# Optimization experiments

Hardware: AMD Instinct MI355X
Metric: run time of the kernel (lower is better)

## Reference

```python
import jax, jax.numpy as jnp
import numpy as np

NUM_CLASSES = 10
OUTPUT_DIM = 128
HIDDEN_DIM = 64


def setup_inputs() -> dict:
    key = jax.random.key(0)
    k1, k2, k3, k4, k5, k6 = jax.random.split(key, 6)
    B, S, F = 16, 4096, 512
    X_support = jax.random.normal(k1, (B, S, F), dtype=jnp.float32)
    y_support = jax.random.randint(k2, (B, S), 0, NUM_CLASSES, dtype=jnp.int32)
    # MLP params: Linear(6, HIDDEN) -> GELU -> Linear(HIDDEN, OUTPUT)
    w1 = jax.random.normal(k3, (6, HIDDEN_DIM), dtype=jnp.float32) * (1.0 / np.sqrt(6.0))
    b1 = jax.random.normal(k4, (HIDDEN_DIM,), dtype=jnp.float32) * 0.01
    w2 = jax.random.normal(k5, (HIDDEN_DIM, OUTPUT_DIM), dtype=jnp.float32) * (1.0 / np.sqrt(HIDDEN_DIM))
    b2 = jax.random.normal(k6, (OUTPUT_DIM,), dtype=jnp.float32) * 0.01
    return {"X_support": X_support, "y_support": y_support,
            "w1": w1, "b1": b1, "w2": w2, "b2": b2}


def _feature_target_stats(X, y):
    """Vectorized equivalent of FeatureTargetStatsEncoder per-(batch,feature) loops.
    X: [B, S, F] float, y: [B, S] int class labels. Returns stats [B, F, 6]."""
    B, S, F = X.shape
    missing_rate = jnp.isnan(X).astype(X.dtype).mean(axis=1)           # [B, F]
    Xc = jnp.nan_to_num(X, nan=0.0)
    gmean = Xc.mean(axis=1)                                            # [B, F]
    variance = Xc.var(axis=1)                                          # biased (unbiased=False)
    absX = jnp.abs(Xc)
    mean_abs = absX.mean(axis=1)
    max_abs = absX.max(axis=1)
    # unique_ratio: count distinct values per (b, f) via sort + diff
    xs = jnp.sort(Xc, axis=1)
    n_unique = 1.0 + (jnp.diff(xs, axis=1) != 0).astype(Xc.dtype).sum(axis=1)
    unique_ratio = n_unique / S
    # classification target score: between-class variance / overall variance
    onehot = jax.nn.one_hot(y, NUM_CLASSES, dtype=Xc.dtype)            # [B, S, C]
    counts = onehot.sum(axis=1)                                        # [B, C]
    csum = jnp.einsum('bsc,bsf->bcf', onehot, Xc)                      # [B, C, F]
    cmean = csum / jnp.maximum(counts, 1.0)[:, :, None]
    dev2 = (cmean - gmean[:, None, :]) ** 2
    between = (counts[:, :, None] * dev2).sum(axis=1) / jnp.maximum(counts.sum(axis=1), 1.0)[:, None]
    target_score = between / jnp.maximum(variance, 1e-6)
    stats = jnp.stack([target_score, missing_rate, unique_ratio,
                       variance, mean_abs, max_abs], axis=-1)          # [B, F, 6]
    return jnp.nan_to_num(stats, nan=0.0, posinf=0.0, neginf=0.0)


def reference(X_support, y_support, w1, b1, w2, b2):
    stats = _feature_target_stats(X_support, y_support)                # [B, F, 6]
    h = jax.nn.gelu(stats @ w1 + b1, approximate=False)               # exact GELU like nn.GELU()
    return h @ w2 + b2                                                 # [B, F, OUTPUT_DIM]
```

## Files before the change

### kernel.cpp

```cpp
#include <hip/hip_runtime.h>
#include <math.h>

#define NS 4096
#define NF 512
#define NB 16
#define NC 10
#define HSIZE 8192
#define HMASK 8191
#define HEMPTY 0xFFFFFFFFu
#define TSR 128
#define TSC 16
#define NSEG 4
#define SEGR (NS / NSEG)
#define WS_P_OFF  1024
#define P2_BYTES (NB * NF * NSEG * 16 * 4)
#define WS_XT_OFF (WS_P_OFF + P2_BYTES)

__device__ __forceinline__ float wave_reduce_add(float v) {
    #pragma unroll
    for (int off = 32; off > 0; off >>= 1) v += __shfl_down(v, off, 64);
    return v;
}

__device__ __forceinline__ unsigned int pat_of(float x) {
    if (x != x) x = 0.f;
    unsigned int p = __float_as_uint(x);
    return (p == 0x80000000u) ? 0u : p;
}

__device__ __forceinline__ float resolve1(unsigned int* hash,
                                          unsigned int s, unsigned int p, unsigned int o) {
    if (o == HEMPTY) return 1.f;
    if (o == p)      return 0.f;
    for (;;) {
        s = (s + 1) & HMASK;
        const unsigned int oo = atomicCAS(&hash[s], HEMPTY, p);
        if (oo == HEMPTY) return 1.f;
        if (oo == p)      return 0.f;
    }
}

__device__ __forceinline__ float hash8(unsigned int* hash, const float4 u, const float4 v) {
    const unsigned int p0 = pat_of(u.x), p1 = pat_of(u.y), p2 = pat_of(u.z), p3 = pat_of(u.w);
    const unsigned int p4 = pat_of(v.x), p5 = pat_of(v.y), p6 = pat_of(v.z), p7 = pat_of(v.w);
    const unsigned int s0 = (p0 * 2654435761u) >> 19, s1 = (p1 * 2654435761u) >> 19;
    const unsigned int s2 = (p2 * 2654435761u) >> 19, s3 = (p3 * 2654435761u) >> 19;
    const unsigned int s4 = (p4 * 2654435761u) >> 19, s5 = (p5 * 2654435761u) >> 19;
    const unsigned int s6 = (p6 * 2654435761u) >> 19, s7 = (p7 * 2654435761u) >> 19;
    const unsigned int o0 = atomicCAS(&hash[s0], HEMPTY, p0);
    const unsigned int o1 = atomicCAS(&hash[s1], HEMPTY, p1);
    const unsigned int o2 = atomicCAS(&hash[s2], HEMPTY, p2);
    const unsigned int o3 = atomicCAS(&hash[s3], HEMPTY, p3);
    const unsigned int o4 = atomicCAS(&hash[s4], HEMPTY, p4);
    const unsigned int o5 = atomicCAS(&hash[s5], HEMPTY, p5);
    const unsigned int o6 = atomicCAS(&hash[s6], HEMPTY, p6);
    const unsigned int o7 = atomicCAS(&hash[s7], HEMPTY, p7);
    float u8 = 0.f;
    u8 += resolve1(hash, s0, p0, o0);
    u8 += resolve1(hash, s1, p1, o1);
    u8 += resolve1(hash, s2, p2, o2);
    u8 += resolve1(hash, s3, p3, o3);
    u8 += resolve1(hash, s4, p4, o4);
    u8 += resolve1(hash, s5, p5, o5);
    u8 += resolve1(hash, s6, p6, o6);
    u8 += resolve1(hash, s7, p7, o7);
    return u8;
}

__launch_bounds__(512, 4)
__global__ void stripe_stats_kernel(const float* __restrict__ X,
                                    float* __restrict__ XT,
                                    const int* __restrict__ y,
                                    float* __restrict__ P2,
                                    int* __restrict__ counts_i) {
    __shared__ float t[TSR][TSC + 1];
    __shared__ int ys[TSR];
    __shared__ int hist[NC];
    const int b   = blockIdx.x;
    const int f0  = blockIdx.y * TSC;
    const int seg = blockIdx.z;
    const int tid = threadIdx.x;
    const bool do_hist = (blockIdx.y == 0);
    if (do_hist && tid < NC) hist[tid] = 0;

    const int lrow = tid >> 2, lq = tid & 3;
    const int col  = tid >> 5, rq = tid & 31;

    const int sbase = seg * SEGR;
    const float* Xb = X + (size_t)b * NS * NF + f0 + lq * 4;
    const int*   yb = y + (size_t)b * NS;

    float sum = 0.f, sumsq = 0.f, sumabs = 0.f, maxabs = 0.f, nancnt = 0.f;
    float csum[NC];
    #pragma unroll
    for (int c = 0; c < NC; c++) csum[c] = 0.f;

    float4 xcur = *(const float4*)(Xb + (size_t)(sbase + lrow) * NF);
    int4 ycur = make_int4(0, 0, 0, 0);
    if (tid < TSR / 4) ycur = *(const int4*)(yb + sbase + tid * 4);

    for (int it = 0; it < SEGR / TSR; ++it) {
        const int s0 = sbase + it * TSR;
        float4 xnext = xcur; int4 ynext = ycur;
        if (it + 1 < SEGR / TSR) {
            xnext = *(const float4*)(Xb + (size_t)(s0 + TSR + lrow) * NF);
            if (tid < TSR / 4) ynext = *(const int4*)(yb + s0 + TSR + tid * 4);
        }
        __syncthreads();
        t[lrow][lq * 4 + 0] = xcur.x; t[lrow][lq * 4 + 1] = xcur.y;
        t[lrow][lq * 4 + 2] = xcur.z; t[lrow][lq * 4 + 3] = xcur.w;
        if (tid < TSR / 4) {
            ys[tid * 4 + 0] = ycur.x; ys[tid * 4 + 1] = ycur.y;
            ys[tid * 4 + 2] = ycur.z; ys[tid * 4 + 3] = ycur.w;
        }
        __syncthreads();
        if (do_hist && tid < TSR) atomicAdd(&hist[ys[tid]], 1);

        #pragma unroll
        for (int j = 0; j < 4; j++) {
            const int r = rq + 32 * j;
            float x = t[r][col];
            const int yc = ys[r];
            if (x != x) { nancnt += 1.f; x = 0.f; }
            sum += x;
            sumsq = fmaf(x, x, sumsq);
            const float a = fabsf(x);
            sumabs += a;
            maxabs = fmaxf(maxabs, a);
            #pragma unroll
            for (int c = 0; c < NC; c++) csum[c] += (yc == c) ? x : 0.f;
        }
        float4 wv;
        wv.x = t[rq * 4 + 0][col]; wv.y = t[rq * 4 + 1][col];
        wv.z = t[rq * 4 + 2][col]; wv.w = t[rq * 4 + 3][col];
        *(float4*)(XT + ((size_t)b * NF + f0 + col) * NS + s0 + rq * 4) = wv;

        xcur = xnext; ycur = ynext;
    }

    float st[15] = { sum, sumsq, sumabs, nancnt, maxabs,
                     csum[0], csum[1], csum[2], csum[3], csum[4],
                     csum[5], csum[6], csum[7], csum[8], csum[9] };
    #pragma unroll
    for (int s = 0; s < 15; s++) {
        float v = st[s];
        #pragma unroll
        for (int off = 16; off > 0; off >>= 1) {
            const float o = __shfl_down(v, off, 32);
            v = (s == 4) ? fmaxf(v, o) : v + o;
        }
        if (rq == 0)
            P2[(((size_t)b * NF + f0 + col) * NSEG + seg) * 16 + s] = v;
    }
    if (do_hist) {
        __syncthreads();
        if (tid < NC) atomicAdd(&counts_i[b * NC + tid], hist[tid]);
    }
}

__launch_bounds__(512, 8)
__global__ void fused_hash_mlp(const float* __restrict__ XT,
                               const float* __restrict__ P2,
                               const int* __restrict__ counts_i,
                               const float* __restrict__ w1,
                               const float* __restrict__ b1,
                               const float* __restrict__ w2,
                               const float* __restrict__ b2,
                               float* __restrict__ out) {
    __shared__ __align__(16) unsigned int hash[HSIZE];

    const int w = blockIdx.x;
    const int g = (w & 7) * 1024 + (w >> 3);
    const int b = g >> 9;
    const int f = g & (NF - 1);
    const int tid = threadIdx.x;
    const int wave = tid >> 6, lane = tid & 63;

    const float4* Xc4 = (const float4*)(XT + ((size_t)b * NF + f) * NS);
    const float4 xa = Xc4[tid];
    const float4 xb = Xc4[512 + tid];

    uint4* h4 = (uint4*)hash;
    const uint4 e4 = make_uint4(HEMPTY, HEMPTY, HEMPTY, HEMPTY);
    #pragma unroll
    for (int i = 0; i < HSIZE / 4 / 512; i++) h4[i * 512 + tid] = e4;
    __syncthreads();

    float uniq = hash8(hash, xa, xb);

    __syncthreads();

    float* r = (float*)hash;
    float* stats_s = r + 32;
    float* h_s = r + 64;

    uniq = wave_reduce_add(uniq);
    if (lane == 0) r[wave] = uniq;
    __syncthreads();

    if (tid == 0) {
        float u = 0.f;
        #pragma unroll
        for (int i = 0; i < 8; i++) u += r[i];
        const float* Pp = P2 + ((size_t)b * NF + f) * (NSEG * 16);
        float S[15];
        #pragma unroll
        for (int s = 0; s < 15; s++) {
            float v0 = Pp[s], v1 = Pp[16 + s], v2 = Pp[32 + s], v3 = Pp[48 + s];
            S[s] = (s == 4) ? fmaxf(fmaxf(v0, v1), fmaxf(v2, v3))
                            : (v0 + v1) + (v2 + v3);
        }
        const float invS = 1.f / (float)NS;
        const float gmean    = S[0] * invS;
        const float variance = fmaxf(S[1] * invS - gmean * gmean, 0.f);
        const float mean_abs = S[2] * invS;
        const float missing  = S[3] * invS;
        const float max_abs  = S[4];
        float between = 0.f;
        #pragma unroll
        for (int c = 0; c < NC; c++) {
            const float cnt = (float)counts_i[b * NC + c];
            const float cm  = S[5 + c] / fmaxf(cnt, 1.f);
            const float d   = cm - gmean;
            between = fmaf(cnt * d, d, between);
        }
        between *= invS;
        const float target = between / fmaxf(variance, 1e-6f);
        float st6[6] = { target, missing, u * invS, variance, mean_abs, max_abs };
        #pragma unroll
        for (int i = 0; i < 6; i++) {
            float v = st6[i];
            if (!(fabsf(v) < INFINITY)) v = 0.f;
            stats_s[i] = v;
        }
    }
    __syncthreads();

    if (tid < 64) {
        float z = b1[tid];
        #pragma unroll
        for (int i = 0; i < 6; i++) z = fmaf(stats_s[i], w1[i * 64 + tid], z);
        h_s[tid] = 0.5f * z * (1.f + erff(z * 0.70710678118654752440f));
    }
    __syncthreads();
    if (tid < 128) {
        float o = b2[tid];
        #pragma unroll
        for (int j = 0; j < 64; j++) o = fmaf(h_s[j], w2[j * 128 + tid], o);
        out[(size_t)g * 128 + tid] = o;
    }
}

__global__ void count_classes_kernel(const int* __restrict__ y, float* __restrict__ counts) {
    __shared__ int hist[NC];
    const int b = blockIdx.x;
    if (threadIdx.x < NC) hist[threadIdx.x] = 0;
    __syncthreads();
    for (int s = threadIdx.x; s < NS; s += blockDim.x)
        atomicAdd(&hist[y[b * NS + s]], 1);
    __syncthreads();
    if (threadIdx.x < NC) counts[b * NC + threadIdx.x] = (float)hist[threadIdx.x];
}

__device__ __forceinline__ float wave_reduce_add64(float v) {
    #pragma unroll
    for (int off = 32; off > 0; off >>= 1) v += __shfl_down(v, off, 64);
    return v;
}
__device__ __forceinline__ float wave_reduce_max64(float v) {
    #pragma unroll
    for (int off = 32; off > 0; off >>= 1) v = fmaxf(v, __shfl_down(v, off, 64));
    return v;
}

__launch_bounds__(256)
__global__ void fused_stats_mlp_kernel(const float* __restrict__ X,
                                       const int* __restrict__ y,
                                       const float* __restrict__ counts,
                                       const float* __restrict__ w1,
                                       const float* __restrict__ b1,
                                       const float* __restrict__ w2,
                                       const float* __restrict__ b2,
                                       float* __restrict__ out) {
    __shared__ unsigned int hash[HSIZE];
    __shared__ float red[4][16];
    __shared__ float stats_s[6];
    __shared__ float h_s[64];

    const int w = blockIdx.x;
    const int g = (w & 7) * 1024 + (w >> 3);
    const int b = g >> 9;
    const int f = g & (NF - 1);
    const int tid = threadIdx.x;

    #pragma unroll
    for (int i = 0; i < HSIZE / 256; i++) hash[tid + i * 256] = HEMPTY;
    __syncthreads();

    const float* Xp = X + (size_t)b * NS * NF + f;
    const int*   yp = y + b * NS;

    float sum = 0.f, sumsq = 0.f, sumabs = 0.f, maxabs = 0.f, nancnt = 0.f, uniq = 0.f;
    float csum[NC];
    #pragma unroll
    for (int c = 0; c < NC; c++) csum[c] = 0.f;

    #pragma unroll
    for (int k0 = 0; k0 < 16; k0 += 8) {
        float xv[8]; int yv[8];
        #pragma unroll
        for (int k = 0; k < 8; k++) {
            const int s = (k0 + k) * 256 + tid;
            xv[k] = Xp[(size_t)s * NF];
            yv[k] = yp[s];
        }
        #pragma unroll
        for (int k = 0; k < 8; k++) {
            float x = xv[k];
            if (x != x) { nancnt += 1.f; x = 0.f; }
            sum += x;
            sumsq = fmaf(x, x, sumsq);
            const float a = fabsf(x);
            sumabs += a;
            maxabs = fmaxf(maxabs, a);
            const int yc = yv[k];
            #pragma unroll
            for (int c = 0; c < NC; c++) csum[c] += (yc == c) ? x : 0.f;
            unsigned int pat = __float_as_uint(x);
            if (pat == 0x80000000u) pat = 0u;
            unsigned int slot = (pat * 2654435761u) >> 19;
            for (;;) {
                const unsigned int old = atomicCAS(&hash[slot], HEMPTY, pat);
                if (old == HEMPTY) { uniq += 1.f; break; }
                if (old == pat) break;
                slot = (slot + 1) & HMASK;
            }
        }
    }

    sum    = wave_reduce_add64(sum);
    sumsq  = wave_reduce_add64(sumsq);
    sumabs = wave_reduce_add64(sumabs);
    nancnt = wave_reduce_add64(nancnt);
    uniq   = wave_reduce_add64(uniq);
    maxabs = wave_reduce_max64(maxabs);
    #pragma unroll
    for (int c = 0; c < NC; c++) csum[c] = wave_reduce_add64(csum[c]);

    const int wave = tid >> 6, lane = tid & 63;
    if (lane == 0) {
        red[wave][0] = sum;    red[wave][1] = sumsq; red[wave][2] = sumabs;
        red[wave][3] = nancnt; red[wave][4] = uniq;  red[wave][5] = maxabs;
        #pragma unroll
        for (int c = 0; c < NC; c++) red[wave][6 + c] = csum[c];
    }
    __syncthreads();

    if (tid == 0) {
        float t[16];
        #pragma unroll
        for (int v = 0; v < 16; v++) t[v] = red[0][v];
        #pragma unroll
        for (int wv = 1; wv < 4; wv++) {
            #pragma unroll
            for (int v = 0; v < 16; v++) {
                if (v == 5) t[v] = fmaxf(t[v], red[wv][v]);
                else        t[v] += red[wv][v];
            }
        }
        const float invS = 1.f / (float)NS;
        const float gmean    = t[0] * invS;
        const float variance = fmaxf(t[1] * invS - gmean * gmean, 0.f);
        const float mean_abs = t[2] * invS;
        const float missing  = t[3] * invS;
        const float n_unique = t[4];
        const float max_abs  = t[5];
        float between = 0.f;
        #pragma unroll
        for (int c = 0; c < NC; c++) {
            const float cnt = counts[b * NC + c];
            const float cm  = t[6 + c] / fmaxf(cnt, 1.f);
            const float d   = cm - gmean;
            between += cnt * d * d;
        }
        between *= invS;
        const float target = between / fmaxf(variance, 1e-6f);
        float st[6] = { target, missing, n_unique * invS, variance, mean_abs, max_abs };
        #pragma unroll
        for (int i = 0; i < 6; i++) {
            float v = st[i];
            if (!(fabsf(v) < INFINITY)) v = 0.f;
            stats_s[i] = v;
        }
    }
    __syncthreads();

    if (tid < 64) {
        float z = b1[tid];
        #pragma unroll
        for (int i = 0; i < 6; i++) z = fmaf(stats_s[i], w1[i * 64 + tid], z);
        h_s[tid] = 0.5f * z * (1.f + erff(z * 0.70710678118654752440f));
    }
    __syncthreads();
    if (tid < 128) {
        float o = b2[tid];
        #pragma unroll
        for (int j = 0; j < 64; j++) o = fmaf(h_s[j], w2[j * 128 + tid], o);
        out[(size_t)g * 128 + tid] = o;
    }
}

extern "C" void kernel_launch(void* const* d_in, const int* in_sizes, int n_in,
                              void* d_out, int out_size, void* d_ws, size_t ws_size,
                              hipStream_t stream) {
    const float* X  = (const float*)d_in[0];
    const int*   y  = (const int*)d_in[1];
    const float* w1 = (const float*)d_in[2];
    const float* b1 = (const float*)d_in[3];
    const float* w2 = (const float*)d_in[4];
    const float* b2 = (const float*)d_in[5];
    float* out = (float*)d_out;

    const size_t xt_bytes = (size_t)NB * NF * NS * sizeof(float);
    if (ws_size >= (size_t)WS_XT_OFF + xt_bytes) {
        int*   counts_i = (int*)d_ws;
        float* P2 = (float*)((char*)d_ws + WS_P_OFF);
        float* XT = (float*)((char*)d_ws + WS_XT_OFF);
        hipMemsetAsync(d_ws, 0, NB * NC * sizeof(int), stream);
        stripe_stats_kernel<<<dim3(NB, NF / TSC, NSEG), 512, 0, stream>>>(
            X, XT, y, P2, counts_i);
        fused_hash_mlp<<<NB * NF, 512, 0, stream>>>(
            XT, P2, counts_i, w1, b1, w2, b2, out);
    } else {
        float* counts = (float*)d_ws;
        count_classes_kernel<<<NB, 256, 0, stream>>>(y, counts);
        fused_stats_mlp_kernel<<<NB * NF, 256, 0, stream>>>(X, y, counts, w1, b1, w2, b2, out);
    }
}
```

Measured before the change: 323.5 us.

## Replace atomicCAS hash insertion with barrier-synchronized write-verify rounds

Distinct-value counting in the fused hash+MLP kernel no longer uses LDS atomicCAS with linear probing. Each round, threads write their patterns to the slot, sync, and check which ones match. Matched threads then elect a unique owner by writing an ID tag, and unmatched elements re-probe with double hashing. This avoids serialized LDS atomics, but each round costs several block-wide barriers, and the number of rounds depends on collision chains.

```diff
diff --git a/kernel.cpp b/kernel.cpp
--- a/kernel.cpp
+++ b/kernel.cpp
@@ -26,45 +26,6 @@
     if (x != x) x = 0.f;
     unsigned int p = __float_as_uint(x);
     return (p == 0x80000000u) ? 0u : p;
-}
-
-__device__ __forceinline__ float resolve1(unsigned int* hash,
-                                          unsigned int s, unsigned int p, unsigned int o) {
-    if (o == HEMPTY) return 1.f;
-    if (o == p)      return 0.f;
-    for (;;) {
-        s = (s + 1) & HMASK;
-        const unsigned int oo = atomicCAS(&hash[s], HEMPTY, p);
-        if (oo == HEMPTY) return 1.f;
-        if (oo == p)      return 0.f;
-    }
-}
-
-__device__ __forceinline__ float hash8(unsigned int* hash, const float4 u, const float4 v) {
-    const unsigned int p0 = pat_of(u.x), p1 = pat_of(u.y), p2 = pat_of(u.z), p3 = pat_of(u.w);
-    const unsigned int p4 = pat_of(v.x), p5 = pat_of(v.y), p6 = pat_of(v.z), p7 = pat_of(v.w);
-    const unsigned int s0 = (p0 * 2654435761u) >> 19, s1 = (p1 * 2654435761u) >> 19;
-    const unsigned int s2 = (p2 * 2654435761u) >> 19, s3 = (p3 * 2654435761u) >> 19;
-    const unsigned int s4 = (p4 * 2654435761u) >> 19, s5 = (p5 * 2654435761u) >> 19;
-    const unsigned int s6 = (p6 * 2654435761u) >> 19, s7 = (p7 * 2654435761u) >> 19;
-    const unsigned int o0 = atomicCAS(&hash[s0], HEMPTY, p0);
-    const unsigned int o1 = atomicCAS(&hash[s1], HEMPTY, p1);
-    const unsigned int o2 = atomicCAS(&hash[s2], HEMPTY, p2);
-    const unsigned int o3 = atomicCAS(&hash[s3], HEMPTY, p3);
-    const unsigned int o4 = atomicCAS(&hash[s4], HEMPTY, p4);
-    const unsigned int o5 = atomicCAS(&hash[s5], HEMPTY, p5);
-    const unsigned int o6 = atomicCAS(&hash[s6], HEMPTY, p6);
-    const unsigned int o7 = atomicCAS(&hash[s7], HEMPTY, p7);
-    float u8 = 0.f;
-    u8 += resolve1(hash, s0, p0, o0);
-    u8 += resolve1(hash, s1, p1, o1);
-    u8 += resolve1(hash, s2, p2, o2);
-    u8 += resolve1(hash, s3, p3, o3);
-    u8 += resolve1(hash, s4, p4, o4);
-    u8 += resolve1(hash, s5, p5, o5);
-    u8 += resolve1(hash, s6, p6, o6);
-    u8 += resolve1(hash, s7, p7, o7);
-    return u8;
 }
 
 __launch_bounds__(512, 4)
@@ -167,7 +128,8 @@
                                const float* __restrict__ w2,
                                const float* __restrict__ b2,
                                float* __restrict__ out) {
-    __shared__ __align__(16) unsigned int hash[HSIZE];
+    __shared__ __align__(16) unsigned int T[HSIZE];
+    __shared__ int anyflag;
 
     const int w = blockIdx.x;
     const int g = (w & 7) * 1024 + (w >> 3);
@@ -180,17 +142,50 @@
     const float4 xa = Xc4[tid];
     const float4 xb = Xc4[512 + tid];
 
-    uint4* h4 = (uint4*)hash;
+    uint4* h4 = (uint4*)T;
     const uint4 e4 = make_uint4(HEMPTY, HEMPTY, HEMPTY, HEMPTY);
     #pragma unroll
     for (int i = 0; i < HSIZE / 4 / 512; i++) h4[i * 512 + tid] = e4;
     __syncthreads();
 
-    float uniq = hash8(hash, xa, xb);
-
-    __syncthreads();
-
-    float* r = (float*)hash;
+    unsigned int pat[8] = { pat_of(xa.x), pat_of(xa.y), pat_of(xa.z), pat_of(xa.w),
+                            pat_of(xb.x), pat_of(xb.y), pat_of(xb.z), pat_of(xb.w) };
+    unsigned int slot[8];
+    #pragma unroll
+    for (int e = 0; e < 8; e++) slot[e] = (pat[e] * 2654435761u) >> 19;
+
+    float uniq = 0.f;
+    int uns = 0xFF;
+    for (;;) {
+        #pragma unroll
+        for (int e = 0; e < 8; e++)
+            if (uns & (1 << e)) T[slot[e]] = pat[e];
+        __syncthreads();
+        int matched = 0;
+        #pragma unroll
+        for (int e = 0; e < 8; e++)
+            if (uns & (1 << e)) matched |= (T[slot[e]] == pat[e]) ? (1 << e) : 0;
+        __syncthreads();
+        if (tid == 0) anyflag = 0;
+        #pragma unroll
+        for (int e = 0; e < 8; e++)
+            if (matched & (1 << e)) T[slot[e]] = 0x7FC00000u | (unsigned)(tid * 8 + e);
+        __syncthreads();
+        #pragma unroll
+        for (int e = 0; e < 8; e++)
+            if (matched & (1 << e))
+                uniq += (T[slot[e]] == (0x7FC00000u | (unsigned)(tid * 8 + e))) ? 1.f : 0.f;
+        uns &= ~matched;
+        #pragma unroll
+        for (int e = 0; e < 8; e++)
+            if (uns & (1 << e))
+                slot[e] = (slot[e] + ((pat[e] & 0x1FFFu) | 1u)) & HMASK;
+        if (uns) anyflag = 1;
+        __syncthreads();
+        if (!anyflag) break;
+    }
+
+    float* r = (float*)T;
     float* stats_s = r + 32;
     float* h_s = r + 64;
 
@@ -262,11 +257,6 @@
     if (threadIdx.x < NC) counts[b * NC + threadIdx.x] = (float)hist[threadIdx.x];
 }
 
-__device__ __forceinline__ float wave_reduce_add64(float v) {
-    #pragma unroll
-    for (int off = 32; off > 0; off >>= 1) v += __shfl_down(v, off, 64);
-    return v;
-}
 __device__ __forceinline__ float wave_reduce_max64(float v) {
     #pragma unroll
     for (int off = 32; off > 0; off >>= 1) v = fmaxf(v, __shfl_down(v, off, 64));
@@ -338,14 +328,14 @@
         }
     }
 
-    sum    = wave_reduce_add64(sum);
-    sumsq  = wave_reduce_add64(sumsq);
-    sumabs = wave_reduce_add64(sumabs);
-    nancnt = wave_reduce_add64(nancnt);
-    uniq   = wave_reduce_add64(uniq);
+    sum    = wave_reduce_add(sum);
+    sumsq  = wave_reduce_add(sumsq);
+    sumabs = wave_reduce_add(sumabs);
+    nancnt = wave_reduce_add(nancnt);
+    uniq   = wave_reduce_add(uniq);
     maxabs = wave_reduce_max64(maxabs);
     #pragma unroll
-    for (int c = 0; c < NC; c++) csum[c] = wave_reduce_add64(csum[c]);
+    for (int c = 0; c < NC; c++) csum[c] = wave_reduce_add(csum[c]);
 
     const int wave = tid >> 6, lane = tid & 63;
     if (lane == 0) {
```

Result: faster. 311.8 us (-3.6%).
